# Performance work log

Hardware: AMD Instinct MI355X
Metric: run time of the kernel (lower is better)

## Reference

```python
import jax, jax.numpy as jnp
import numpy as np

SCORE_THR = 0.3   # SSD.score_threshold
NMS_THR = 0.6     # SSD.nms_threshold
TOP_K = 100       # fixed candidate count per class (jit-friendly padded NMS)
CODER_W = (10.0, 10.0, 5.0, 5.0)  # SSD.coder_weights
B, A, C = 32, 8732, 81


def setup_inputs() -> dict:
    key = jax.random.key(0)
    k1, k2, k3 = jax.random.split(key, 3)
    class_logits = jax.random.normal(k1, (B, A, C), jnp.float32)
    box_regression = jax.random.normal(k2, (B, A, 4), jnp.float32)
    u = jax.random.uniform(k3, (A, 4), jnp.float32)
    centers = u[:, :2]                      # cy, cx in [0,1]
    sizes = 0.05 + 0.45 * u[:, 2:]          # h, w in [0.05, 0.5]
    priors = jnp.concatenate([centers, sizes], axis=-1)  # [A,4] (cy,cx,h,w)
    return {"class_logits": class_logits, "box_regression": box_regression, "priors": priors}


def decode_boxes(rel, priors):
    # rel: [...,A,4] codes (ty,tx,th,tw); priors: [A,4] (cy,cx,h,w); standard TF SSD box coder
    ty = rel[..., 0] / CODER_W[0]
    tx = rel[..., 1] / CODER_W[1]
    th = rel[..., 2] / CODER_W[2]
    tw = rel[..., 3] / CODER_W[3]
    cy = ty * priors[..., 2] + priors[..., 0]
    cx = tx * priors[..., 3] + priors[..., 1]
    h = jnp.exp(th) * priors[..., 2]
    w = jnp.exp(tw) * priors[..., 3]
    # corners (ymin, xmin, ymax, xmax)
    return jnp.stack([cy - h / 2, cx - w / 2, cy + h / 2, cx + w / 2], axis=-1)


def _iou_matrix(b):
    # b: [K,4] corners -> [K,K] pairwise IoU
    area = jnp.clip(b[:, 2] - b[:, 0], 0) * jnp.clip(b[:, 3] - b[:, 1], 0)
    tl = jnp.maximum(b[:, None, :2], b[None, :, :2])
    br = jnp.minimum(b[:, None, 2:], b[None, :, 2:])
    wh = jnp.clip(br - tl, 0)
    inter = wh[..., 0] * wh[..., 1]
    return inter / (area[:, None] + area[None, :] - inter + 1e-9)


def _nms_one_class(boxes, probs):
    # boxes: [A,4], probs: [A] -> padded [TOP_K,5] (box + score, zeros where suppressed)
    valid_all = probs > SCORE_THR
    masked = jnp.where(valid_all, probs, -1.0)
    top, idx = jax.lax.top_k(masked, TOP_K)          # sorted descending
    b = boxes[idx]                                    # [TOP_K,4]
    valid = top > SCORE_THR
    iou = _iou_matrix(jax.lax.stop_gradient(b))       # NMS selection is non-differentiable
    rng = jnp.arange(TOP_K)

    def body(i, keep):
        cur = keep[i] & valid[i]
        sup = (iou[i] > NMS_THR) & (rng > i)
        return jnp.where(cur, keep & ~sup, keep)

    keep = jax.lax.fori_loop(0, TOP_K, body, jnp.ones((TOP_K,), bool)) & valid
    out_b = jnp.where(keep[:, None], b, 0.0)
    out_s = jnp.where(keep, top, 0.0)
    return jnp.concatenate([out_b, out_s[:, None]], axis=-1)  # [TOP_K,5]


def reference(class_logits, box_regression, priors):
    scores = jax.nn.sigmoid(class_logits)             # [B,A,C]
    boxes = decode_boxes(box_regression, priors)      # [B,A,4]
    fg = scores[..., 1:]                              # skip background class 0 -> [B,A,C-1]
    per_class = jax.vmap(_nms_one_class, in_axes=(None, 1))   # over classes
    per_image = jax.vmap(per_class, in_axes=(0, 0))           # over batch
    return per_image(boxes, fg)                       # [B, C-1, TOP_K, 5]
```

## Files before the change

### kernel.cpp

```cpp
#include <hip/hip_runtime.h>
#include <math.h>

#define A_N   8732
#define C_N   81
#define B_N   32
#define NCLS  80
#define NTASK (B_N * NCLS)
#define TOPK  100
#define NTHR  256
#define CAND  512
#define ACH   128
#define NCH   ((A_N + ACH - 1) / ACH)
#define LCAP  16
#define CPAD  16
#define THR_LOGIT (-0.8472978603872034)
#define XFIX  2.0f

#define OFF_SB0    0
#define OFF_SB1    800
#define OFF_SB2    1600
#define OFF_SB3    2400
#define OFF_SAREA  3200
#define OFF_KEEPW  4000
#define OFF_HIST   0
#define OFF_CAND   8192
#define OFF_FB0    8192
#define OFF_FB1    8592
#define OFF_FB2    8992
#define OFF_FB3    9392
#define OFF_FAREA  9792
#define OFF_FSC    10192
#define OFF_SVAL   10592
#define OFF_SSEL   12288
#define OFF_SUP    13088
#define OFF_WT4    14688
#define OFF_SCAL   14704
#define SMEM_SZ    14720

__device__ __forceinline__ unsigned mapf(float x) {
    unsigned b = __float_as_uint(x);
    return b ^ ((b & 0x80000000u) ? 0xFFFFFFFFu : 0x80000000u);
}
__device__ __forceinline__ float unmapf(unsigned u) {
    unsigned b = (u & 0x80000000u) ? (u ^ 0x80000000u) : ~u;
    return __uint_as_float(b);
}

__device__ __forceinline__ void dec64(const float4 r4, const float4 p4,
                                      double* bx, double* area) {
    double ty = (double)r4.x / 10.0, tx = (double)r4.y / 10.0;
    double th = (double)r4.z / 5.0,  tw = (double)r4.w / 5.0;
    double cy = ty * (double)p4.z + (double)p4.x;
    double cx = tx * (double)p4.w + (double)p4.y;
    double hh = exp(th) * (double)p4.z;
    double ww = exp(tw) * (double)p4.w;
    bx[0] = cy - hh / 2.0; bx[1] = cx - ww / 2.0;
    bx[2] = cy + hh / 2.0; bx[3] = cx + ww / 2.0;
    double e0 = bx[2] - bx[0]; if (e0 < 0.0) e0 = 0.0;
    double e1 = bx[3] - bx[1]; if (e1 < 0.0) e1 = 0.0;
    *area = e0 * e1;
}

__global__ __launch_bounds__(NTHR) void scatter_cand_kernel(
    const float* __restrict__ logits,
    unsigned long long* __restrict__ gcand,
    unsigned* __restrict__ gcountP)
{
    __shared__ unsigned long long llist[NCLS * LCAP];
    __shared__ unsigned lcnt[NCLS];
    __shared__ unsigned sbase[NCLS];

    const int b  = blockIdx.x / NCH;
    const int ck = blockIdx.x % NCH;
    const int a0 = ck * ACH;
    const int an = min(ACH, A_N - a0);
    const int tid = threadIdx.x;

    for (int i = tid; i < NCLS; i += NTHR) lcnt[i] = 0;
    __syncthreads();

    const size_t E0 = (size_t)C_N * ((size_t)b * A_N + a0);
    const unsigned NE = (unsigned)(an * C_N);
    const size_t F0 = E0 >> 2;
    const size_t F1 = (E0 + NE + 3) >> 2;
    const float4* src4 = (const float4*)logits;

    for (size_t f = F0 + tid; f < F1; f += NTHR) {
        float4 v = src4[f];
        size_t e = f * 4;
        float xs[4] = { v.x, v.y, v.z, v.w };
        #pragma unroll
        for (int k = 0; k < 4; ++k, ++e) {
            if (e >= E0 && e < E0 + NE && xs[k] >= XFIX) {
                unsigned rel = (unsigned)(e - E0);
                unsigned ar = rel / (unsigned)C_N;
                unsigned ch = rel - ar * (unsigned)C_N;
                if (ch > 0) {
                    int t = (int)ch - 1;
                    unsigned a = (unsigned)a0 + ar;
                    unsigned long long key =
                        ((unsigned long long)mapf(xs[k]) << 32) | (unsigned)(~a);
                    unsigned pos = atomicAdd(&lcnt[t], 1u);
                    if (pos < LCAP) {
                        llist[t * LCAP + pos] = key;
                    } else {
                        int task = b * NCLS + t;
                        unsigned p = atomicAdd(&gcountP[task * CPAD], 1u);
                        if (p < CAND) gcand[(size_t)task * CAND + p] = key;
                    }
                }
            }
        }
    }
    __syncthreads();

    if (tid < NCLS) {
        unsigned n = lcnt[tid]; if (n > LCAP) n = LCAP;
        sbase[tid] = n ? atomicAdd(&gcountP[(b * NCLS + tid) * CPAD], n) : 0u;
        lcnt[tid] = n;
    }
    __syncthreads();

    for (int i = tid; i < NCLS * LCAP; i += NTHR) {
        int t = i >> 4, s = i & (LCAP - 1);
        if ((unsigned)s < lcnt[t]) {
            unsigned dst = sbase[t] + (unsigned)s;
            if (dst < CAND)
                gcand[(size_t)(b * NCLS + t) * CAND + dst] = llist[i];
        }
    }
}

__global__ __launch_bounds__(NTHR) void ssd_nms_kernel(
    const float* __restrict__ logits,
    const unsigned long long* __restrict__ gcand,
    const unsigned* __restrict__ gcountP,
    const float* __restrict__ boxreg,
    const float* __restrict__ priors,
    float* __restrict__ out)
{
    const int task = blockIdx.x;
    const int b = task / NCLS;
    const int c = task % NCLS;
    const int tid = threadIdx.x;

    __shared__ __align__(16) char smem[SMEM_SZ];
    unsigned* hist = (unsigned*)(smem + OFF_HIST);
    unsigned long long* cand = (unsigned long long*)(smem + OFF_CAND);
    unsigned long long* ssel = (unsigned long long*)(smem + OFF_SSEL);
    unsigned* wt4 = (unsigned*)(smem + OFF_WT4);
    int* scal = (int*)(smem + OFF_SCAL);
    double* sb0 = (double*)(smem + OFF_SB0);
    double* sb1 = (double*)(smem + OFF_SB1);
    double* sb2 = (double*)(smem + OFF_SB2);
    double* sb3 = (double*)(smem + OFF_SB3);
    double* sarea = (double*)(smem + OFF_SAREA);
    float* fb0 = (float*)(smem + OFF_FB0);
    float* fb1 = (float*)(smem + OFF_FB1);
    float* fb2 = (float*)(smem + OFF_FB2);
    float* fb3 = (float*)(smem + OFF_FB3);
    float* farea = (float*)(smem + OFF_FAREA);
    float* fscore = (float*)(smem + OFF_FSC);
    int* svalid = (int*)(smem + OFF_SVAL);
    unsigned long long (*supmask)[2] = (unsigned long long (*)[2])(smem + OFF_SUP);
    unsigned long long* keepw = (unsigned long long*)(smem + OFF_KEEPW);

    const float* lg = logits + ((size_t)b * A_N * C_N) + (c + 1);

    if (tid < TOPK) ssel[tid] = 0ull;
    if (tid == 0) { scal[0] = 0; scal[1] = 1; }

    const int count = (int)gcountP[task * CPAD];
    int M;
    if (count >= TOPK && count <= CAND) {
        M = count;
        const unsigned long long* lst = gcand + (size_t)task * CAND;
        for (int i = tid; i < M; i += NTHR) cand[i] = lst[i];
    } else {
        for (int k = tid; k < 2048; k += NTHR) hist[k] = 0;
        __syncthreads();
        for (int a = tid; a < A_N; a += NTHR) {
            float x = lg[(size_t)a * C_N];
            if ((double)x > THR_LOGIT) atomicAdd(&hist[mapf(x) >> 21], 1u);
        }
        __syncthreads();
        {
            unsigned s = 0;
            #pragma unroll
            for (int k = 0; k < 8; ++k) s += hist[tid * 8 + k];
            unsigned incl = s;
            int lane = tid & 63;
            #pragma unroll
            for (int off = 1; off < 64; off <<= 1) {
                unsigned v = __shfl_down(incl, off);
                if (lane + off < 64) incl += v;
            }
            if (lane == 0) wt4[tid >> 6] = incl;
            __syncthreads();
            unsigned hi = 0;
            #pragma unroll
            for (int w = 0; w < 4; ++w) if (w > (tid >> 6)) hi += wt4[w];
            unsigned excl = hi + (incl - s);
            if (excl < TOPK && excl + s >= TOPK) {
                unsigned running = excl;
                #pragma unroll
                for (int k = 7; k >= 0; --k) {
                    running += hist[tid * 8 + k];
                    if (running >= TOPK) { scal[1] = (int)(((unsigned)(tid * 8 + k)) << 21); break; }
                }
            }
        }
        __syncthreads();
        const unsigned cutoff = (unsigned)scal[1];
        for (int a = tid; a < A_N; a += NTHR) {
            float x = lg[(size_t)a * C_N];
            if ((double)x > THR_LOGIT) {
                unsigned u = mapf(x);
                if (u >= cutoff) {
                    int p = atomicAdd(&scal[0], 1);
                    if (p < CAND) cand[p] = ((unsigned long long)u << 32) | (unsigned)(~(unsigned)a);
                }
            }
        }
        __syncthreads();
        M = min(scal[0], CAND);
    }
    {
        int Mr = (M + 7) & ~7;
        for (int i = M + tid; i < Mr; i += NTHR) cand[i] = 0ull;
    }
    __syncthreads();

    {
        int Mr = (M + 7) & ~7;
        for (int i = tid; i < Mr; i += NTHR) {
            unsigned long long mykey = cand[i];
            int rank = 0;
            #pragma unroll 8
            for (int j = 0; j < Mr; ++j) rank += (cand[j] > mykey) ? 1 : 0;
            if (mykey != 0ull && rank < TOPK) ssel[rank] = mykey;
        }
    }
    __syncthreads();

    if (tid < TOPK) {
        unsigned long long key = ssel[tid];
        int valid = (key != 0ull);
        double bx[4] = {0.0, 0.0, 0.0, 0.0}, ar = 0.0;
        float sc = 0.f;
        if (valid) {
            int a = (int)(~(unsigned)key);
            float x = unmapf((unsigned)(key >> 32));
            sc = 1.0f / (1.0f + __expf(-x));
            float4 r4 = *(const float4*)(boxreg + ((size_t)b * A_N + a) * 4);
            float4 p4 = *(const float4*)(priors + (size_t)a * 4);
            dec64(r4, p4, bx, &ar);
        }
        sb0[tid] = bx[0]; sb1[tid] = bx[1]; sb2[tid] = bx[2]; sb3[tid] = bx[3];
        sarea[tid] = ar;
        fb0[tid] = (float)bx[0]; fb1[tid] = (float)bx[1];
        fb2[tid] = (float)bx[2]; fb3[tid] = (float)bx[3];
        farea[tid] = (float)ar;
        fscore[tid] = sc;
        svalid[tid] = valid;
    }
    __syncthreads();

    if (tid < 2 * TOPK) {
        int i = tid >> 1, w = tid & 1;
        unsigned long long m = 0;
        if (svalid[i]) {
            float i0 = fb0[i], i1 = fb1[i], i2 = fb2[i], i3 = fb3[i], ia = farea[i];
            int jbase = w * 64;
            int jend = min(jbase + 64, TOPK);
            int jstart = (jbase > i + 1) ? jbase : (i + 1);
            for (int j = jstart; j < jend; ++j) {
                float tl0 = fmaxf(i0, fb0[j]);
                float tl1 = fmaxf(i1, fb1[j]);
                float br0 = fminf(i2, fb2[j]);
                float br1 = fminf(i3, fb3[j]);
                float wh0 = fmaxf(br0 - tl0, 0.0f);
                float wh1 = fmaxf(br1 - tl1, 0.0f);
                float inter = wh0 * wh1;
                float denom = (ia + farea[j]) - inter;
                bool sup = inter > 0.6004f * denom;
                bool amb = !sup && (inter > 0.5996f * denom) && (inter > 0.0f);
                if (amb) {
                    double tl0d = fmax(sb0[i], sb0[j]);
                    double tl1d = fmax(sb1[i], sb1[j]);
                    double br0d = fmin(sb2[i], sb2[j]);
                    double br1d = fmin(sb3[i], sb3[j]);
                    double wh0d = br0d - tl0d; if (wh0d < 0.0) wh0d = 0.0;
                    double wh1d = br1d - tl1d; if (wh1d < 0.0) wh1d = 0.0;
                    double interd = wh0d * wh1d;
                    double denomd = ((sarea[i] + sarea[j]) - interd) + 1e-9;
                    sup = interd > 0.6 * denomd;
                }
                if (sup) m |= 1ull << (j - jbase);
            }
        }
        supmask[i][w] = m;
    }
    __syncthreads();

    if (tid == 0) {
        unsigned long long kp0 = ~0ull, kp1 = ~0ull;
        for (int i = 0; i < TOPK; ++i) {
            bool kb = (i < 64) ? ((kp0 >> i) & 1ull) : ((kp1 >> (i - 64)) & 1ull);
            if (kb && svalid[i]) { kp0 &= ~supmask[i][0]; kp1 &= ~supmask[i][1]; }
        }
        keepw[0] = kp0; keepw[1] = kp1;
    }
    __syncthreads();

    if (tid < TOPK) {
        bool kb = (tid < 64) ? ((keepw[0] >> tid) & 1ull)
                             : ((keepw[1] >> (tid - 64)) & 1ull);
        bool kp = kb && (svalid[tid] != 0);
        size_t base = ((size_t)task * TOPK + tid) * 5;
        out[base + 0] = kp ? fb0[tid] : 0.0f;
        out[base + 1] = kp ? fb1[tid] : 0.0f;
        out[base + 2] = kp ? fb2[tid] : 0.0f;
        out[base + 3] = kp ? fb3[tid] : 0.0f;
        out[base + 4] = kp ? fscore[tid] : 0.0f;
    }
}

__global__ __launch_bounds__(NTHR) void ssd_nms_fallback(
    const float* __restrict__ logits,
    const float* __restrict__ boxreg,
    const float* __restrict__ priors,
    float* __restrict__ out)
{
    const int task = blockIdx.x;
    const int b = task / NCLS;
    const int c = task % NCLS;
    const int tid = threadIdx.x;

    __shared__ unsigned hist[2048];
    __shared__ unsigned wt4[4];
    __shared__ unsigned long long cand[CAND];
    __shared__ unsigned long long ssel[TOPK];
    __shared__ double sb0[TOPK], sb1[TOPK], sb2[TOPK], sb3[TOPK], sarea[TOPK];
    __shared__ float fb0[TOPK], fb1[TOPK], fb2[TOPK], fb3[TOPK];
    __shared__ float farea[TOPK], fscore[TOPK];
    __shared__ int svalid[TOPK];
    __shared__ unsigned long long supmask[TOPK][2];
    __shared__ unsigned long long keepw[2];
    __shared__ int scal[2];

    const float* lg = logits + ((size_t)b * A_N * C_N) + (c + 1);

    for (int k = tid; k < 2048; k += NTHR) hist[k] = 0;
    for (int i = tid; i < CAND; i += NTHR) cand[i] = 0ull;
    if (tid < TOPK) ssel[tid] = 0ull;
    if (tid == 0) { scal[0] = 0; scal[1] = 1; }
    __syncthreads();

    for (int a = tid; a < A_N; a += NTHR) {
        float x = lg[(size_t)a * C_N];
        if ((double)x > THR_LOGIT) atomicAdd(&hist[mapf(x) >> 21], 1u);
    }
    __syncthreads();
    {
        unsigned s = 0;
        #pragma unroll
        for (int k = 0; k < 8; ++k) s += hist[tid * 8 + k];
        unsigned incl = s;
        int lane = tid & 63;
        #pragma unroll
        for (int off = 1; off < 64; off <<= 1) {
            unsigned v = __shfl_down(incl, off);
            if (lane + off < 64) incl += v;
        }
        if (lane == 0) wt4[tid >> 6] = incl;
        __syncthreads();
        unsigned hi = 0;
        #pragma unroll
        for (int w = 0; w < 4; ++w) if (w > (tid >> 6)) hi += wt4[w];
        unsigned excl = hi + (incl - s);
        if (excl < TOPK && excl + s >= TOPK) {
            unsigned running = excl;
            #pragma unroll
            for (int k = 7; k >= 0; --k) {
                running += hist[tid * 8 + k];
                if (running >= TOPK) { scal[1] = (int)(((unsigned)(tid * 8 + k)) << 21); break; }
            }
        }
    }
    __syncthreads();
    const unsigned cutoff = (unsigned)scal[1];

    for (int a = tid; a < A_N; a += NTHR) {
        float x = lg[(size_t)a * C_N];
        if ((double)x > THR_LOGIT) {
            unsigned u = mapf(x);
            if (u >= cutoff) {
                int p = atomicAdd(&scal[0], 1);
                if (p < CAND) cand[p] = ((unsigned long long)u << 32) | (unsigned)(~(unsigned)a);
            }
        }
    }
    __syncthreads();
    const int M = min(scal[0], CAND);
    {
        int Mr = (M + 7) & ~7;
        for (int i = tid; i < Mr; i += NTHR) {
            unsigned long long mykey = cand[i];
            int rank = 0;
            for (int j = 0; j < Mr; ++j) rank += (cand[j] > mykey) ? 1 : 0;
            if (mykey != 0ull && rank < TOPK) ssel[rank] = mykey;
        }
    }
    __syncthreads();
    if (tid < TOPK) {
        unsigned long long key = ssel[tid];
        int valid = (key != 0ull);
        double bx[4] = {0.0, 0.0, 0.0, 0.0}, ar = 0.0;
        float sc = 0.f;
        if (valid) {
            int a = (int)(~(unsigned)key);
            float x = unmapf((unsigned)(key >> 32));
            sc = 1.0f / (1.0f + __expf(-x));
            float4 r4 = *(const float4*)(boxreg + ((size_t)b * A_N + a) * 4);
            float4 p4 = *(const float4*)(priors + (size_t)a * 4);
            dec64(r4, p4, bx, &ar);
        }
        sb0[tid] = bx[0]; sb1[tid] = bx[1]; sb2[tid] = bx[2]; sb3[tid] = bx[3];
        sarea[tid] = ar;
        fb0[tid] = (float)bx[0]; fb1[tid] = (float)bx[1];
        fb2[tid] = (float)bx[2]; fb3[tid] = (float)bx[3];
        farea[tid] = (float)ar; fscore[tid] = sc; svalid[tid] = valid;
    }
    __syncthreads();
    if (tid < 2 * TOPK) {
        int i = tid >> 1, w = tid & 1;
        unsigned long long m = 0;
        if (svalid[i]) {
            float i0=fb0[i], i1=fb1[i], i2=fb2[i], i3=fb3[i], ia=farea[i];
            int jbase = w * 64, jend = min(jbase + 64, TOPK);
            int jstart = (jbase > i + 1) ? jbase : (i + 1);
            for (int j = jstart; j < jend; ++j) {
                float tl0=fmaxf(i0,fb0[j]), tl1=fmaxf(i1,fb1[j]);
                float br0=fminf(i2,fb2[j]), br1=fminf(i3,fb3[j]);
                float wh0=fmaxf(br0-tl0,0.f), wh1=fmaxf(br1-tl1,0.f);
                float inter=wh0*wh1, denom=(ia+farea[j])-inter;
                bool sup = inter > 0.6004f*denom;
                bool amb = !sup && (inter > 0.5996f*denom) && (inter > 0.f);
                if (amb) {
                    double tl0d = fmax(sb0[i], sb0[j]);
                    double tl1d = fmax(sb1[i], sb1[j]);
                    double br0d = fmin(sb2[i], sb2[j]);
                    double br1d = fmin(sb3[i], sb3[j]);
                    double wh0d = br0d - tl0d; if (wh0d < 0.0) wh0d = 0.0;
                    double wh1d = br1d - tl1d; if (wh1d < 0.0) wh1d = 0.0;
                    double interd = wh0d * wh1d;
                    sup = interd > 0.6 * (((sarea[i] + sarea[j]) - interd) + 1e-9);
                }
                if (sup) m |= 1ull << (j - jbase);
            }
        }
        supmask[i][w] = m;
    }
    __syncthreads();
    if (tid == 0) {
        unsigned long long kp0 = ~0ull, kp1 = ~0ull;
        for (int i = 0; i < TOPK; ++i) {
            bool kb = (i < 64) ? ((kp0 >> i) & 1ull) : ((kp1 >> (i - 64)) & 1ull);
            if (kb && svalid[i]) { kp0 &= ~supmask[i][0]; kp1 &= ~supmask[i][1]; }
        }
        keepw[0] = kp0; keepw[1] = kp1;
    }
    __syncthreads();
    if (tid < TOPK) {
        bool kb = (tid < 64) ? ((keepw[0] >> tid) & 1ull)
                             : ((keepw[1] >> (tid - 64)) & 1ull);
        bool kp = kb && (svalid[tid] != 0);
        size_t base = ((size_t)task * TOPK + tid) * 5;
        out[base + 0] = kp ? fb0[tid] : 0.0f;
        out[base + 1] = kp ? fb1[tid] : 0.0f;
        out[base + 2] = kp ? fb2[tid] : 0.0f;
        out[base + 3] = kp ? fb3[tid] : 0.0f;
        out[base + 4] = kp ? fscore[tid] : 0.0f;
    }
}

extern "C" void kernel_launch(void* const* d_in, const int* in_sizes, int n_in,
                              void* d_out, int out_size, void* d_ws, size_t ws_size,
                              hipStream_t stream) {
    const float* logits = (const float*)d_in[0];
    const float* boxreg = (const float*)d_in[1];
    const float* priors = (const float*)d_in[2];
    float* out = (float*)d_out;

    const size_t cand_bytes  = (size_t)NTASK * CAND * sizeof(unsigned long long);
    const size_t count_bytes = (size_t)NTASK * CPAD * sizeof(unsigned);
    if (ws_size >= cand_bytes + count_bytes) {
        unsigned long long* gcand = (unsigned long long*)d_ws;
        unsigned* gcountP = (unsigned*)((char*)d_ws + cand_bytes);
        hipMemsetAsync(gcountP, 0, count_bytes, stream);
        scatter_cand_kernel<<<dim3(B_N * NCH), dim3(NTHR), 0, stream>>>(
            logits, gcand, gcountP);
        ssd_nms_kernel<<<dim3(NTASK), dim3(NTHR), 0, stream>>>(
            logits, gcand, gcountP, boxreg, priors, out);
    } else {
        ssd_nms_fallback<<<dim3(NTASK), dim3(NTHR), 0, stream>>>(
            logits, boxreg, priors, out);
    }
}
```

Before: 91.70 us.

## Map one NMS task per wavefront, four tasks per block, drop block barriers

```diff
diff --git a/kernel.cpp b/kernel.cpp
--- a/kernel.cpp
+++ b/kernel.cpp
@@ -16,27 +16,6 @@
 #define THR_LOGIT (-0.8472978603872034)
 #define XFIX  2.0f
 
-#define OFF_SB0    0
-#define OFF_SB1    800
-#define OFF_SB2    1600
-#define OFF_SB3    2400
-#define OFF_SAREA  3200
-#define OFF_KEEPW  4000
-#define OFF_HIST   0
-#define OFF_CAND   8192
-#define OFF_FB0    8192
-#define OFF_FB1    8592
-#define OFF_FB2    8992
-#define OFF_FB3    9392
-#define OFF_FAREA  9792
-#define OFF_FSC    10192
-#define OFF_SVAL   10592
-#define OFF_SSEL   12288
-#define OFF_SUP    13088
-#define OFF_WT4    14688
-#define OFF_SCAL   14704
-#define SMEM_SZ    14720
-
 __device__ __forceinline__ unsigned mapf(float x) {
     unsigned b = __float_as_uint(x);
     return b ^ ((b & 0x80000000u) ? 0xFFFFFFFFu : 0x80000000u);
@@ -87,6 +66,8 @@
 
     for (size_t f = F0 + tid; f < F1; f += NTHR) {
         float4 v = src4[f];
+        float mx = fmaxf(fmaxf(v.x, v.y), fmaxf(v.z, v.w));
+        if (mx < XFIX) continue;
         size_t e = f * 4;
         float xs[4] = { v.x, v.y, v.z, v.w };
         #pragma unroll
@@ -131,7 +112,7 @@
     }
 }
 
-__global__ __launch_bounds__(NTHR) void ssd_nms_kernel(
+__global__ __launch_bounds__(NTHR) void ssd_nms_wave4(
     const float* __restrict__ logits,
     const unsigned long long* __restrict__ gcand,
     const unsigned* __restrict__ gcountP,
@@ -139,190 +120,219 @@
     const float* __restrict__ priors,
     float* __restrict__ out)
 {
-    const int task = blockIdx.x;
+    __shared__ unsigned long long candL[4][CAND];
+    __shared__ unsigned long long sselL[4][TOPK];
+    __shared__ double sbL[4][4][TOPK];
+    __shared__ double saL[4][TOPK];
+    __shared__ float4 fbL[4][TOPK];
+    __shared__ float  faL[4][TOPK];
+
+    const int w = threadIdx.x >> 6;
+    const int l = threadIdx.x & 63;
+    const int task = blockIdx.x * 4 + w;
     const int b = task / NCLS;
     const int c = task % NCLS;
-    const int tid = threadIdx.x;
-
-    __shared__ __align__(16) char smem[SMEM_SZ];
-    unsigned* hist = (unsigned*)(smem + OFF_HIST);
-    unsigned long long* cand = (unsigned long long*)(smem + OFF_CAND);
-    unsigned long long* ssel = (unsigned long long*)(smem + OFF_SSEL);
-    unsigned* wt4 = (unsigned*)(smem + OFF_WT4);
-    int* scal = (int*)(smem + OFF_SCAL);
-    double* sb0 = (double*)(smem + OFF_SB0);
-    double* sb1 = (double*)(smem + OFF_SB1);
-    double* sb2 = (double*)(smem + OFF_SB2);
-    double* sb3 = (double*)(smem + OFF_SB3);
-    double* sarea = (double*)(smem + OFF_SAREA);
-    float* fb0 = (float*)(smem + OFF_FB0);
-    float* fb1 = (float*)(smem + OFF_FB1);
-    float* fb2 = (float*)(smem + OFF_FB2);
-    float* fb3 = (float*)(smem + OFF_FB3);
-    float* farea = (float*)(smem + OFF_FAREA);
-    float* fscore = (float*)(smem + OFF_FSC);
-    int* svalid = (int*)(smem + OFF_SVAL);
-    unsigned long long (*supmask)[2] = (unsigned long long (*)[2])(smem + OFF_SUP);
-    unsigned long long* keepw = (unsigned long long*)(smem + OFF_KEEPW);
-
     const float* lg = logits + ((size_t)b * A_N * C_N) + (c + 1);
 
-    if (tid < TOPK) ssel[tid] = 0ull;
-    if (tid == 0) { scal[0] = 0; scal[1] = 1; }
-
+    sselL[w][l] = 0ull;
+    if (l < TOPK - 64) sselL[w][64 + l] = 0ull;
+
+    int M = 0;
     const int count = (int)gcountP[task * CPAD];
-    int M;
     if (count >= TOPK && count <= CAND) {
         M = count;
         const unsigned long long* lst = gcand + (size_t)task * CAND;
-        for (int i = tid; i < M; i += NTHR) cand[i] = lst[i];
+        #pragma unroll
+        for (int k = 0; k < CAND / 64; ++k) {
+            int idx = l + k * 64;
+            if (idx < M) candL[w][idx] = lst[idx];
+        }
     } else {
-        for (int k = tid; k < 2048; k += NTHR) hist[k] = 0;
-        __syncthreads();
-        for (int a = tid; a < A_N; a += NTHR) {
-            float x = lg[(size_t)a * C_N];
-            if ((double)x > THR_LOGIT) atomicAdd(&hist[mapf(x) >> 21], 1u);
-        }
-        __syncthreads();
+        unsigned cut = 1u;
         {
-            unsigned s = 0;
+            int nv = 0;
+            for (int a = l; a < A_N; a += 64) {
+                float x = lg[(size_t)a * C_N];
+                if ((double)x > THR_LOGIT) nv++;
+            }
             #pragma unroll
-            for (int k = 0; k < 8; ++k) s += hist[tid * 8 + k];
-            unsigned incl = s;
-            int lane = tid & 63;
-            #pragma unroll
-            for (int off = 1; off < 64; off <<= 1) {
-                unsigned v = __shfl_down(incl, off);
-                if (lane + off < 64) incl += v;
-            }
-            if (lane == 0) wt4[tid >> 6] = incl;
-            __syncthreads();
-            unsigned hi = 0;
-            #pragma unroll
-            for (int w = 0; w < 4; ++w) if (w > (tid >> 6)) hi += wt4[w];
-            unsigned excl = hi + (incl - s);
-            if (excl < TOPK && excl + s >= TOPK) {
-                unsigned running = excl;
-                #pragma unroll
-                for (int k = 7; k >= 0; --k) {
-                    running += hist[tid * 8 + k];
-                    if (running >= TOPK) { scal[1] = (int)(((unsigned)(tid * 8 + k)) << 21); break; }
+            for (int off = 32; off; off >>= 1) nv += __shfl_down(nv, off);
+            nv = __shfl(nv, 0);
+            if (nv > CAND) {
+                unsigned lo = 1u, hi = 0xFFFFFFFFu;
+                for (int it = 0; it < 34; ++it) {
+                    unsigned mid = lo + ((hi - lo) >> 1);
+                    if (mid == lo) break;
+                    int cm = 0;
+                    for (int a = l; a < A_N; a += 64) {
+                        float x = lg[(size_t)a * C_N];
+                        if ((double)x > THR_LOGIT && mapf(x) >= mid) cm++;
+                    }
+                    #pragma unroll
+                    for (int off = 32; off; off >>= 1) cm += __shfl_down(cm, off);
+                    cm = __shfl(cm, 0);
+                    if (cm >= TOPK) lo = mid; else hi = mid;
                 }
-            }
-        }
-        __syncthreads();
-        const unsigned cutoff = (unsigned)scal[1];
-        for (int a = tid; a < A_N; a += NTHR) {
-            float x = lg[(size_t)a * C_N];
-            if ((double)x > THR_LOGIT) {
-                unsigned u = mapf(x);
-                if (u >= cutoff) {
-                    int p = atomicAdd(&scal[0], 1);
-                    if (p < CAND) cand[p] = ((unsigned long long)u << 32) | (unsigned)(~(unsigned)a);
+                cut = lo;
+            }
+        }
+        int cnt2 = 0;
+        for (int a0i = 0; a0i < A_N; a0i += 64) {
+            int a = a0i + l;
+            bool pr = false; unsigned long long key = 0ull;
+            if (a < A_N) {
+                float x = lg[(size_t)a * C_N];
+                if ((double)x > THR_LOGIT) {
+                    unsigned u = mapf(x);
+                    if (u >= cut) {
+                        pr = true;
+                        key = ((unsigned long long)u << 32) | (unsigned)(~(unsigned)a);
+                    }
                 }
             }
-        }
-        __syncthreads();
-        M = min(scal[0], CAND);
-    }
+            unsigned long long mk = __ballot(pr);
+            if (pr) {
+                int pos = cnt2 + (int)__popcll(mk & ((1ull << l) - 1ull));
+                if (pos < CAND) candL[w][pos] = key;
+            }
+            cnt2 += (int)__popcll(mk);
+        }
+        M = min(cnt2, CAND);
+    }
+    const int Mr = (M + 3) & ~3;
+    for (int idx = M + l; idx < Mr; idx += 64) candL[w][idx] = 0ull;
+
+    unsigned long long myk[CAND / 64];
+    int rk[CAND / 64];
+    const int Kr = (Mr + 63) >> 6;
+    #pragma unroll
+    for (int k = 0; k < CAND / 64; ++k) {
+        int idx = l + k * 64;
+        myk[k] = (idx < Mr) ? candL[w][idx] : 0ull;
+        rk[k] = 0;
+    }
+    for (int j = 0; j < Mr; j += 4) {
+        unsigned long long c0 = candL[w][j + 0];
+        unsigned long long c1 = candL[w][j + 1];
+        unsigned long long c2 = candL[w][j + 2];
+        unsigned long long c3 = candL[w][j + 3];
+        for (int k = 0; k < Kr; ++k) {
+            rk[k] += (c0 > myk[k]) ? 1 : 0;
+            rk[k] += (c1 > myk[k]) ? 1 : 0;
+            rk[k] += (c2 > myk[k]) ? 1 : 0;
+            rk[k] += (c3 > myk[k]) ? 1 : 0;
+        }
+    }
+    #pragma unroll
+    for (int k = 0; k < CAND / 64; ++k)
+        if (myk[k] != 0ull && rk[k] < TOPK) sselL[w][rk[k]] = myk[k];
+
+    unsigned long long keyA = sselL[w][l];
+    unsigned long long keyB = (l < TOPK - 64) ? sselL[w][64 + l] : 0ull;
+    float A0 = 0, A1 = 0, A2 = 0, A3 = 0, arA = 0, scA = 0;
+    float B0 = 0, B1 = 0, B2 = 0, B3 = 0, arB = 0, scB = 0;
     {
-        int Mr = (M + 7) & ~7;
-        for (int i = M + tid; i < Mr; i += NTHR) cand[i] = 0ull;
-    }
-    __syncthreads();
-
-    {
-        int Mr = (M + 7) & ~7;
-        for (int i = tid; i < Mr; i += NTHR) {
-            unsigned long long mykey = cand[i];
-            int rank = 0;
-            #pragma unroll 8
-            for (int j = 0; j < Mr; ++j) rank += (cand[j] > mykey) ? 1 : 0;
-            if (mykey != 0ull && rank < TOPK) ssel[rank] = mykey;
-        }
-    }
-    __syncthreads();
-
-    if (tid < TOPK) {
-        unsigned long long key = ssel[tid];
-        int valid = (key != 0ull);
         double bx[4] = {0.0, 0.0, 0.0, 0.0}, ar = 0.0;
-        float sc = 0.f;
-        if (valid) {
-            int a = (int)(~(unsigned)key);
-            float x = unmapf((unsigned)(key >> 32));
-            sc = 1.0f / (1.0f + __expf(-x));
+        if (keyA) {
+            int a = (int)(~(unsigned)keyA);
+            float x = unmapf((unsigned)(keyA >> 32));
+            scA = 1.0f / (1.0f + __expf(-x));
             float4 r4 = *(const float4*)(boxreg + ((size_t)b * A_N + a) * 4);
             float4 p4 = *(const float4*)(priors + (size_t)a * 4);
             dec64(r4, p4, bx, &ar);
         }
-        sb0[tid] = bx[0]; sb1[tid] = bx[1]; sb2[tid] = bx[2]; sb3[tid] = bx[3];
-        sarea[tid] = ar;
-        fb0[tid] = (float)bx[0]; fb1[tid] = (float)bx[1];
-        fb2[tid] = (float)bx[2]; fb3[tid] = (float)bx[3];
-        farea[tid] = (float)ar;
-        fscore[tid] = sc;
-        svalid[tid] = valid;
-    }
-    __syncthreads();
-
-    if (tid < 2 * TOPK) {
-        int i = tid >> 1, w = tid & 1;
-        unsigned long long m = 0;
-        if (svalid[i]) {
-            float i0 = fb0[i], i1 = fb1[i], i2 = fb2[i], i3 = fb3[i], ia = farea[i];
-            int jbase = w * 64;
-            int jend = min(jbase + 64, TOPK);
-            int jstart = (jbase > i + 1) ? jbase : (i + 1);
-            for (int j = jstart; j < jend; ++j) {
-                float tl0 = fmaxf(i0, fb0[j]);
-                float tl1 = fmaxf(i1, fb1[j]);
-                float br0 = fminf(i2, fb2[j]);
-                float br1 = fminf(i3, fb3[j]);
-                float wh0 = fmaxf(br0 - tl0, 0.0f);
-                float wh1 = fmaxf(br1 - tl1, 0.0f);
-                float inter = wh0 * wh1;
-                float denom = (ia + farea[j]) - inter;
-                bool sup = inter > 0.6004f * denom;
-                bool amb = !sup && (inter > 0.5996f * denom) && (inter > 0.0f);
-                if (amb) {
-                    double tl0d = fmax(sb0[i], sb0[j]);
-                    double tl1d = fmax(sb1[i], sb1[j]);
-                    double br0d = fmin(sb2[i], sb2[j]);
-                    double br1d = fmin(sb3[i], sb3[j]);
-                    double wh0d = br0d - tl0d; if (wh0d < 0.0) wh0d = 0.0;
-                    double wh1d = br1d - tl1d; if (wh1d < 0.0) wh1d = 0.0;
-                    double interd = wh0d * wh1d;
-                    double denomd = ((sarea[i] + sarea[j]) - interd) + 1e-9;
-                    sup = interd > 0.6 * denomd;
-                }
-                if (sup) m |= 1ull << (j - jbase);
-            }
-        }
-        supmask[i][w] = m;
-    }
-    __syncthreads();
-
-    if (tid == 0) {
-        unsigned long long kp0 = ~0ull, kp1 = ~0ull;
-        for (int i = 0; i < TOPK; ++i) {
-            bool kb = (i < 64) ? ((kp0 >> i) & 1ull) : ((kp1 >> (i - 64)) & 1ull);
-            if (kb && svalid[i]) { kp0 &= ~supmask[i][0]; kp1 &= ~supmask[i][1]; }
-        }
-        keepw[0] = kp0; keepw[1] = kp1;
-    }
-    __syncthreads();
-
-    if (tid < TOPK) {
-        bool kb = (tid < 64) ? ((keepw[0] >> tid) & 1ull)
-                             : ((keepw[1] >> (tid - 64)) & 1ull);
-        bool kp = kb && (svalid[tid] != 0);
-        size_t base = ((size_t)task * TOPK + tid) * 5;
-        out[base + 0] = kp ? fb0[tid] : 0.0f;
-        out[base + 1] = kp ? fb1[tid] : 0.0f;
-        out[base + 2] = kp ? fb2[tid] : 0.0f;
-        out[base + 3] = kp ? fb3[tid] : 0.0f;
-        out[base + 4] = kp ? fscore[tid] : 0.0f;
+        sbL[w][0][l] = bx[0]; sbL[w][1][l] = bx[1];
+        sbL[w][2][l] = bx[2]; sbL[w][3][l] = bx[3];
+        saL[w][l] = ar;
+        A0 = (float)bx[0]; A1 = (float)bx[1]; A2 = (float)bx[2]; A3 = (float)bx[3];
+        arA = (float)ar;
+        fbL[w][l] = make_float4(A0, A1, A2, A3); faL[w][l] = arA;
+    }
+    if (l < TOPK - 64) {
+        double bx[4] = {0.0, 0.0, 0.0, 0.0}, ar = 0.0;
+        if (keyB) {
+            int a = (int)(~(unsigned)keyB);
+            float x = unmapf((unsigned)(keyB >> 32));
+            scB = 1.0f / (1.0f + __expf(-x));
+            float4 r4 = *(const float4*)(boxreg + ((size_t)b * A_N + a) * 4);
+            float4 p4 = *(const float4*)(priors + (size_t)a * 4);
+            dec64(r4, p4, bx, &ar);
+        }
+        sbL[w][0][64 + l] = bx[0]; sbL[w][1][64 + l] = bx[1];
+        sbL[w][2][64 + l] = bx[2]; sbL[w][3][64 + l] = bx[3];
+        saL[w][64 + l] = ar;
+        B0 = (float)bx[0]; B1 = (float)bx[1]; B2 = (float)bx[2]; B3 = (float)bx[3];
+        arB = (float)ar;
+        fbL[w][64 + l] = make_float4(B0, B1, B2, B3); faL[w][64 + l] = arB;
+    }
+    const unsigned long long v0 = __ballot(keyA != 0ull);
+    const unsigned long long v1 = __ballot((l < TOPK - 64) && keyB != 0ull);
+
+    auto pairSup = [&](float i0, float i1, float i2, float i3, float ia,
+                       int irow, int j) -> bool {
+        float4 bj = fbL[w][j]; float aj = faL[w][j];
+        float tl0 = fmaxf(i0, bj.x), tl1 = fmaxf(i1, bj.y);
+        float br0 = fminf(i2, bj.z), br1 = fminf(i3, bj.w);
+        float wh0 = fmaxf(br0 - tl0, 0.f), wh1 = fmaxf(br1 - tl1, 0.f);
+        float inter = wh0 * wh1;
+        float denom = (ia + aj) - inter;
+        bool sup = inter > 0.6004f * denom;
+        bool amb = !sup && (inter > 0.5996f * denom) && (inter > 0.f);
+        if (amb) {
+            double tl0d = fmax(sbL[w][0][irow], sbL[w][0][j]);
+            double tl1d = fmax(sbL[w][1][irow], sbL[w][1][j]);
+            double br0d = fmin(sbL[w][2][irow], sbL[w][2][j]);
+            double br1d = fmin(sbL[w][3][irow], sbL[w][3][j]);
+            double wh0d = br0d - tl0d; if (wh0d < 0.0) wh0d = 0.0;
+            double wh1d = br1d - tl1d; if (wh1d < 0.0) wh1d = 0.0;
+            double interd = wh0d * wh1d;
+            sup = interd > 0.6 * (((saL[w][irow] + saL[w][j]) - interd) + 1e-9);
+        }
+        return sup;
+    };
+
+    unsigned long long mA0 = 0, mA1 = 0, mB0 = 0, mB1 = 0;
+    if (l < 50) {
+        for (int j = l + 1; j < TOPK; ++j)
+            if (pairSup(A0, A1, A2, A3, arA, l, j)) {
+                if (j < 64) mA0 |= 1ull << j; else mA1 |= 1ull << (j - 64);
+            }
+        int rB = 99 - l;
+        float4 bi = fbL[w][rB]; float ai = faL[w][rB];
+        for (int j = rB + 1; j < TOPK; ++j)
+            if (pairSup(bi.x, bi.y, bi.z, bi.w, ai, rB, j)) {
+                if (j < 64) mB0 |= 1ull << j; else mB1 |= 1ull << (j - 64);
+            }
+    }
+
+    unsigned long long kp0 = ~0ull, kp1 = (1ull << (TOPK - 64)) - 1ull;
+    for (int i = 0; i < TOPK; ++i) {
+        bool low = (i < 50);
+        int src = low ? i : 99 - i;
+        unsigned long long m0 = low ? __shfl(mA0, src) : __shfl(mB0, src);
+        unsigned long long m1 = low ? __shfl(mA1, src) : __shfl(mB1, src);
+        bool kb = (i < 64) ? ((kp0 >> i) & 1ull) : ((kp1 >> (i - 64)) & 1ull);
+        bool vb = (i < 64) ? ((v0 >> i) & 1ull) : ((v1 >> (i - 64)) & 1ull);
+        if (kb && vb) { kp0 &= ~m0; kp1 &= ~m1; }
+    }
+
+    {
+        bool keepA = ((kp0 >> l) & 1ull) && (keyA != 0ull);
+        size_t baseA = ((size_t)task * TOPK + l) * 5;
+        out[baseA + 0] = keepA ? A0 : 0.0f;
+        out[baseA + 1] = keepA ? A1 : 0.0f;
+        out[baseA + 2] = keepA ? A2 : 0.0f;
+        out[baseA + 3] = keepA ? A3 : 0.0f;
+        out[baseA + 4] = keepA ? scA : 0.0f;
+        if (l < TOPK - 64) {
+            bool keepB = ((kp1 >> l) & 1ull) && (keyB != 0ull);
+            size_t baseB = ((size_t)task * TOPK + 64 + l) * 5;
+            out[baseB + 0] = keepB ? B0 : 0.0f;
+            out[baseB + 1] = keepB ? B1 : 0.0f;
+            out[baseB + 2] = keepB ? B2 : 0.0f;
+            out[baseB + 3] = keepB ? B3 : 0.0f;
+            out[baseB + 4] = keepB ? scB : 0.0f;
+        }
     }
 }
 
@@ -501,7 +511,7 @@
         hipMemsetAsync(gcountP, 0, count_bytes, stream);
         scatter_cand_kernel<<<dim3(B_N * NCH), dim3(NTHR), 0, stream>>>(
             logits, gcand, gcountP);
-        ssd_nms_kernel<<<dim3(NTASK), dim3(NTHR), 0, stream>>>(
+        ssd_nms_wave4<<<dim3(NTASK / 4), dim3(NTHR), 0, stream>>>(
             logits, gcand, gcountP, boxreg, priors, out);
     } else {
         ssd_nms_fallback<<<dim3(NTASK), dim3(NTHR), 0, stream>>>(
```

Result: slower. 155.3 us (+69.4%).

## Use bitonic sort for small candidate sets and wavefront-parallel NMS keep scan

Applied to the files above, without the earlier changes.

```diff
diff --git a/kernel.cpp b/kernel.cpp
--- a/kernel.cpp
+++ b/kernel.cpp
@@ -167,15 +167,27 @@
 
     const float* lg = logits + ((size_t)b * A_N * C_N) + (c + 1);
 
+    const unsigned long long* lst = gcand + (size_t)task * CAND;
+    unsigned long long pre0 = lst[tid];
+    unsigned long long pre1 = lst[tid + NTHR];
+    const int count = (int)gcountP[task * CPAD];
+
     if (tid < TOPK) ssel[tid] = 0ull;
     if (tid == 0) { scal[0] = 0; scal[1] = 1; }
 
-    const int count = (int)gcountP[task * CPAD];
+    const bool optim = (count >= TOPK && count <= CAND);
+    const bool useSort = optim && (count <= 256);
     int M;
-    if (count >= TOPK && count <= CAND) {
+    if (optim) {
         M = count;
-        const unsigned long long* lst = gcand + (size_t)task * CAND;
-        for (int i = tid; i < M; i += NTHR) cand[i] = lst[i];
+        if (useSort) {
+            cand[tid] = (tid < M) ? pre0 : 0ull;
+        } else {
+            if (tid < M) cand[tid] = pre0;
+            if (tid + NTHR < M) cand[tid + NTHR] = pre1;
+            int Mr = (M + 7) & ~7;
+            for (int i = M + tid; i < Mr; i += NTHR) cand[i] = 0ull;
+        }
     } else {
         for (int k = tid; k < 2048; k += NTHR) hist[k] = 0;
         __syncthreads();
@@ -224,14 +236,27 @@
         }
         __syncthreads();
         M = min(scal[0], CAND);
-    }
-    {
         int Mr = (M + 7) & ~7;
         for (int i = M + tid; i < Mr; i += NTHR) cand[i] = 0ull;
     }
     __syncthreads();
 
-    {
+    if (useSort) {
+        for (int k2 = 2; k2 <= 256; k2 <<= 1) {
+            for (int j = k2 >> 1; j > 0; j >>= 1) {
+                int t = tid;
+                int ixj = t ^ j;
+                if (ixj > t) {
+                    unsigned long long x0 = cand[t], x1 = cand[ixj];
+                    bool descSeg = ((t & k2) == 0);
+                    bool sw = descSeg ? (x0 < x1) : (x0 > x1);
+                    if (sw) { cand[t] = x1; cand[ixj] = x0; }
+                }
+                __syncthreads();
+            }
+        }
+        if (tid < TOPK) ssel[tid] = cand[tid];
+    } else {
         int Mr = (M + 7) & ~7;
         for (int i = tid; i < Mr; i += NTHR) {
             unsigned long long mykey = cand[i];
@@ -303,13 +328,27 @@
     }
     __syncthreads();
 
-    if (tid == 0) {
+    if (tid < 64) {
+        unsigned long long m0A = supmask[tid][0], m1A = supmask[tid][1];
+        int vA = svalid[tid];
+        unsigned long long m0B = 0, m1B = 0; int vB = 0;
+        if (tid < TOPK - 64) {
+            m0B = supmask[64 + tid][0]; m1B = supmask[64 + tid][1];
+            vB = svalid[64 + tid];
+        }
+        unsigned long long v0b = __ballot(vA != 0);
+        unsigned long long v1b = __ballot(vB != 0);
         unsigned long long kp0 = ~0ull, kp1 = ~0ull;
         for (int i = 0; i < TOPK; ++i) {
-            bool kb = (i < 64) ? ((kp0 >> i) & 1ull) : ((kp1 >> (i - 64)) & 1ull);
-            if (kb && svalid[i]) { kp0 &= ~supmask[i][0]; kp1 &= ~supmask[i][1]; }
-        }
-        keepw[0] = kp0; keepw[1] = kp1;
+            bool low = (i < 64);
+            int src = low ? i : (i - 64);
+            unsigned long long m0 = low ? __shfl(m0A, src) : __shfl(m0B, src);
+            unsigned long long m1 = low ? __shfl(m1A, src) : __shfl(m1B, src);
+            bool kb = low ? ((kp0 >> i) & 1ull) : ((kp1 >> (i - 64)) & 1ull);
+            bool vb = low ? ((v0b >> i) & 1ull) : ((v1b >> (i - 64)) & 1ull);
+            if (kb && vb) { kp0 &= ~m0; kp1 &= ~m1; }
+        }
+        if (tid == 0) { keepw[0] = kp0; keepw[1] = kp1; }
     }
     __syncthreads();
 
```

Measured after the change: 99.21 us. 1.08x slower.

## Early-out float4 groups in scatter, raise prefilter, wave-parallel NMS resolve

Applied to the files above, without the earlier changes.

```diff
diff --git a/kernel.cpp b/kernel.cpp
--- a/kernel.cpp
+++ b/kernel.cpp
@@ -14,7 +14,7 @@
 #define LCAP  16
 #define CPAD  16
 #define THR_LOGIT (-0.8472978603872034)
-#define XFIX  2.0f
+#define XFIX  2.1f
 
 #define OFF_SB0    0
 #define OFF_SB1    800
@@ -79,20 +79,20 @@
     for (int i = tid; i < NCLS; i += NTHR) lcnt[i] = 0;
     __syncthreads();
 
-    const size_t E0 = (size_t)C_N * ((size_t)b * A_N + a0);
-    const unsigned NE = (unsigned)(an * C_N);
-    const size_t F0 = E0 >> 2;
-    const size_t F1 = (E0 + NE + 3) >> 2;
-    const float4* src4 = (const float4*)logits;
-
-    for (size_t f = F0 + tid; f < F1; f += NTHR) {
+    const unsigned NE4 = (unsigned)(an * C_N) / 4u;
+    const float4* src4 = (const float4*)logits
+                       + ((size_t)C_N * ((size_t)b * A_N + a0)) / 4;
+
+    for (unsigned f = tid; f < NE4; f += NTHR) {
         float4 v = src4[f];
-        size_t e = f * 4;
+        float mx = fmaxf(fmaxf(v.x, v.y), fmaxf(v.z, v.w));
+        if (mx < XFIX) continue;
+        unsigned e = f * 4u;
         float xs[4] = { v.x, v.y, v.z, v.w };
         #pragma unroll
-        for (int k = 0; k < 4; ++k, ++e) {
-            if (e >= E0 && e < E0 + NE && xs[k] >= XFIX) {
-                unsigned rel = (unsigned)(e - E0);
+        for (int k = 0; k < 4; ++k) {
+            if (xs[k] >= XFIX) {
+                unsigned rel = e + (unsigned)k;
                 unsigned ar = rel / (unsigned)C_N;
                 unsigned ch = rel - ar * (unsigned)C_N;
                 if (ch > 0) {
@@ -303,13 +303,27 @@
     }
     __syncthreads();
 
-    if (tid == 0) {
+    if (tid < 64) {
+        unsigned long long m0A = supmask[tid][0], m1A = supmask[tid][1];
+        int vA = svalid[tid];
+        unsigned long long m0B = 0, m1B = 0; int vB = 0;
+        if (tid < TOPK - 64) {
+            m0B = supmask[64 + tid][0]; m1B = supmask[64 + tid][1];
+            vB = svalid[64 + tid];
+        }
+        unsigned long long v0b = __ballot(vA != 0);
+        unsigned long long v1b = __ballot(vB != 0);
         unsigned long long kp0 = ~0ull, kp1 = ~0ull;
         for (int i = 0; i < TOPK; ++i) {
-            bool kb = (i < 64) ? ((kp0 >> i) & 1ull) : ((kp1 >> (i - 64)) & 1ull);
-            if (kb && svalid[i]) { kp0 &= ~supmask[i][0]; kp1 &= ~supmask[i][1]; }
-        }
-        keepw[0] = kp0; keepw[1] = kp1;
+            bool low = (i < 64);
+            int src = low ? i : (i - 64);
+            unsigned long long m0 = low ? __shfl(m0A, src) : __shfl(m0B, src);
+            unsigned long long m1 = low ? __shfl(m1A, src) : __shfl(m1B, src);
+            bool kb = low ? ((kp0 >> i) & 1ull) : ((kp1 >> (i - 64)) & 1ull);
+            bool vb = low ? ((v0b >> i) & 1ull) : ((v1b >> (i - 64)) & 1ull);
+            if (kb && vb) { kp0 &= ~m0; kp1 &= ~m1; }
+        }
+        if (tid == 0) { keepw[0] = kp0; keepw[1] = kp1; }
     }
     __syncthreads();
 
```

Measured after the change: 96.19 us. 4.9% more time.
